# Performance work log

Measured on AMD Instinct MI355X. Metric: run time of the kernel, lower is better.

The kernel has to match this reference:

```python
import jax, jax.numpy as jnp
import numpy as np

N_NODES = 100000
N_EDGES = 800000
IN_FEATS = 128
HIDDEN = 64
SCALE = 0.5 ** 0.5  # sqrt(0.5) residual scale
BN_EPS = 1e-5


def setup_inputs() -> dict:
    key = jax.random.key(0)
    ks = jax.random.split(key, 12)
    return {
        "src": jax.random.randint(ks[0], (N_EDGES,), 0, N_NODES, dtype=jnp.int64)
        if jax.config.jax_enable_x64 else jax.random.randint(ks[0], (N_EDGES,), 0, N_NODES),
        "dst": jax.random.randint(ks[1], (N_EDGES,), 0, N_NODES),
        "x": jax.random.normal(ks[2], (N_NODES, IN_FEATS), dtype=jnp.float32),
        "fc_w": jax.random.normal(ks[3], (IN_FEATS, HIDDEN), dtype=jnp.float32) * 0.05,
        "fc_b": jax.random.normal(ks[4], (HIDDEN,), dtype=jnp.float32) * 0.05,
        "w1": jax.random.normal(ks[5], (HIDDEN, HIDDEN), dtype=jnp.float32) * 0.05,
        "b1": jax.random.normal(ks[6], (HIDDEN,), dtype=jnp.float32) * 0.05,
        "w2": jax.random.normal(ks[7], (HIDDEN, HIDDEN), dtype=jnp.float32) * 0.05,
        "b2": jax.random.normal(ks[8], (HIDDEN,), dtype=jnp.float32) * 0.05,
        "gamma": jax.random.normal(ks[9], (HIDDEN,), dtype=jnp.float32) * 0.05 + 1.0,
        "beta": jax.random.normal(ks[10], (HIDDEN,), dtype=jnp.float32) * 0.05,
    }


def _graph_conv(h, w, b, src, dst, norm_src, norm_dst, n_nodes):
    # DGL GraphConv, norm='both': y = D_in^{-1/2} A D_out^{-1/2} (h W) + b
    h = h @ w                                   # [N, H]
    m = h[src] * norm_src[:, None]              # gather + src-degree norm, [E, H]
    agg = jax.ops.segment_sum(m, dst, num_segments=n_nodes)  # scatter-add, [N, H]
    return agg * norm_dst[:, None] + b


def reference(src, dst, x, fc_w, fc_b, w1, b1, w2, b2, gamma, beta):
    n_nodes = x.shape[0]
    ones_e = jnp.ones(src.shape[0], dtype=x.dtype)
    deg_out = jnp.clip(jax.ops.segment_sum(ones_e, src, num_segments=n_nodes), 1.0)
    deg_in = jnp.clip(jax.ops.segment_sum(ones_e, dst, num_segments=n_nodes), 1.0)
    norm_src = (deg_out ** -0.5)[src]           # per-edge source normalization
    norm_dst = deg_in ** -0.5                   # per-node destination normalization

    h = x @ fc_w + fc_b                          # fc: [N, H]
    h = (h + _graph_conv(h, w1, b1, src, dst, norm_src, norm_dst, n_nodes)) * SCALE
    h = (h + _graph_conv(h, w2, b2, src, dst, norm_src, norm_dst, n_nodes)) * SCALE

    # BatchNorm1d (training-mode batch statistics over nodes, biased variance)
    mu = h.mean(axis=0)
    var = ((h - mu) ** 2).mean(axis=0)
    h = (h - mu) * jax.lax.rsqrt(var + BN_EPS) * gamma + beta
    return h
```

## Files before the change

### kernel.cpp

```cpp
#include <hip/hip_runtime.h>

#define HIDDEN 64
#define INFEAT 128
#define SCALE_C 0.70710678118654752f
#define BN_EPS 1e-5f
#define AGG_GRID 2048
#define RED_BLK 32

__device__ __forceinline__ int rli(int v, int l){ return __builtin_amdgcn_readlane(v, l); }
__device__ __forceinline__ float rlf(float v, int l){
  return __int_as_float(__builtin_amdgcn_readlane(__float_as_int(v), l));
}

template<int KDIM, bool ADDB, bool FUSET>
__device__ __forceinline__ void gemm_body(int bid, const float* __restrict__ X,
    const float* __restrict__ W, const float* __restrict__ B,
    float* __restrict__ Y, const float* __restrict__ W2, float* __restrict__ T, int N)
{
  __shared__ float smem[64 * 65];
  const int tid  = threadIdx.x;
  const int lane = tid & 63;
  const int wid  = __builtin_amdgcn_readfirstlane(tid >> 6);
  const int c0 = wid * 16;
  const int base = bid * 64;
  const int gnode = base + lane;

  float acc[16];
  #pragma unroll
  for (int c = 0; c < 16; ++c) acc[c] = ADDB ? B[c0 + c] : 0.f;

  constexpr int NCHUNK = KDIM / 32;
  #pragma unroll 1
  for (int ck = 0; ck < NCHUNK; ++ck){
    __syncthreads();
    #pragma unroll
    for (int i = 0; i < 2; ++i){
      int f  = i * 256 + tid;
      int nd = f >> 3;
      int kq = f & 7;
      float4 v = make_float4(0.f, 0.f, 0.f, 0.f);
      if (base + nd < N)
        v = *(const float4*)(X + (size_t)(base + nd) * KDIM + ck * 32 + kq * 4);
      float* p = &smem[nd * 65 + kq * 4];
      p[0] = v.x; p[1] = v.y; p[2] = v.z; p[3] = v.w;
    }
    __syncthreads();
    const float* wrow = W + (size_t)ck * 32 * HIDDEN + c0;
    #pragma unroll
    for (int k = 0; k < 32; ++k){
      float xv = smem[lane * 65 + k];
      #pragma unroll
      for (int c = 0; c < 16; ++c)
        acc[c] = fmaf(xv, wrow[k * HIDDEN + c], acc[c]);
    }
  }

  if (gnode < N){
    float4* yp = (float4*)(Y + (size_t)gnode * HIDDEN + c0);
    #pragma unroll
    for (int j = 0; j < 4; ++j)
      yp[j] = make_float4(acc[4*j], acc[4*j+1], acc[4*j+2], acc[4*j+3]);
  }

  if constexpr (FUSET){
    __syncthreads();
    #pragma unroll
    for (int c = 0; c < 16; ++c) smem[lane * 65 + c0 + c] = acc[c];
    __syncthreads();
    float tacc[16];
    #pragma unroll
    for (int c = 0; c < 16; ++c) tacc[c] = 0.f;
    const float* w2r = W2 + c0;
    #pragma unroll
    for (int k = 0; k < 64; ++k){
      float hv = smem[lane * 65 + k];
      #pragma unroll
      for (int c = 0; c < 16; ++c)
        tacc[c] = fmaf(hv, w2r[k * HIDDEN + c], tacc[c]);
    }
    if (gnode < N){
      float4* tp = (float4*)(T + (size_t)gnode * HIDDEN + c0);
      #pragma unroll
      for (int j = 0; j < 4; ++j)
        tp[j] = make_float4(tacc[4*j], tacc[4*j+1], tacc[4*j+2], tacc[4*j+3]);
    }
  }
}

__device__ __forceinline__ int role_gemm_idx(int b, int GB, int TOT, int& histIdx){
  int fb  = (int)(((long)b * GB) / TOT);
  int fb1 = (int)(((long)(b + 1) * GB) / TOT);
  histIdx = b - fb;
  return (fb1 > fb) ? fb : -1;
}

__global__ __launch_bounds__(256) void k_mega1(const int* __restrict__ dst,
    int* __restrict__ degI, int* __restrict__ rank, int E,
    const float* __restrict__ x, const float* __restrict__ fc_w,
    const float* __restrict__ fc_b, float* __restrict__ h,
    const float* __restrict__ w1, float* __restrict__ t, int N, int GB, int TOT){
  int hIdx;
  int g = role_gemm_idx(blockIdx.x, GB, TOT, hIdx);
  if (g >= 0) gemm_body<INFEAT, true, true>(g, x, fc_w, fc_b, h, w1, t, N);
  else {
    int e0 = hIdx * 1024 + threadIdx.x;
    #pragma unroll
    for (int i = 0; i < 4; ++i){
      int e = e0 + i * 256;
      if (e < E) rank[e] = atomicAdd(&degI[dst[e]], 1);
    }
  }
}

__global__ __launch_bounds__(256) void k_place(const int* __restrict__ src,
    const int* __restrict__ dst, const int* __restrict__ rank,
    const int* __restrict__ rp, int* __restrict__ cs, int* __restrict__ degO, int E){
  int e0 = blockIdx.x * 1024 + threadIdx.x;
  #pragma unroll
  for (int i = 0; i < 4; ++i){
    int e = e0 + i * 256;
    if (e < E){
      int s = src[e];
      cs[rp[dst[e]] + rank[e]] = s;
      atomicAdd(&degO[s], 1);
    }
  }
}

__global__ __launch_bounds__(256) void k_gemm64(const float* __restrict__ X,
    const float* __restrict__ W, float* __restrict__ Y, int N){
  gemm_body<HIDDEN, false, false>(blockIdx.x, X, W, nullptr, Y, nullptr, nullptr, N);
}

__global__ void k_scan1(const int* __restrict__ deg, int* __restrict__ bsum, int N){
  __shared__ int sh[256];
  int t = threadIdx.x;
  int i = blockIdx.x * 256 + t;
  sh[t] = (i < N) ? deg[i] : 0;
  __syncthreads();
  for (int ofs = 128; ofs > 0; ofs >>= 1){
    if (t < ofs) sh[t] += sh[t + ofs];
    __syncthreads();
  }
  if (t == 0) bsum[blockIdx.x] = sh[0];
}

__global__ void k_scan2(int* __restrict__ bsum, int NB){
  __shared__ int sh[512];
  int t = threadIdx.x;
  int v = (t < NB) ? bsum[t] : 0;
  sh[t] = v;
  __syncthreads();
  for (int ofs = 1; ofs < 512; ofs <<= 1){
    int u = (t >= ofs) ? sh[t - ofs] : 0;
    __syncthreads();
    sh[t] += u;
    __syncthreads();
  }
  if (t < NB) bsum[t] = sh[t] - v;
}

__global__ void k_scan3(const int* __restrict__ degI, const int* __restrict__ bofs,
                        int* __restrict__ rp, float* __restrict__ norm_in, int N, int E){
  __shared__ int sh[256];
  int t = threadIdx.x;
  int i = blockIdx.x * 256 + t;
  int v = (i < N) ? degI[i] : 0;
  sh[t] = v;
  __syncthreads();
  for (int ofs = 1; ofs < 256; ofs <<= 1){
    int u = (t >= ofs) ? sh[t - ofs] : 0;
    __syncthreads();
    sh[t] += u;
    __syncthreads();
  }
  if (i < N){
    int excl = sh[t] - v + bofs[blockIdx.x];
    rp[i] = excl;
    if (i == N - 1) rp[N] = E;
    norm_in[i] = rsqrtf((float)max(v, 1));
  }
}

template<bool PRE>
__device__ __forceinline__ float gather_row(const int* __restrict__ rp,
    const int* __restrict__ cs, const float* __restrict__ t,
    const int* __restrict__ degO, int n, int lane){
  const int start = rp[n], end = rp[n + 1];
  float acc = 0.f;
  for (int j0 = start; j0 < end; j0 += 64){
    int cnt = end - j0; if (cnt > 64) cnt = 64;
    int sidx = (j0 + lane < end) ? cs[j0 + lane] : 0;
    int d = 0;
    for (; d + 8 <= cnt; d += 8){
      int a0 = rli(sidx, d),   a1 = rli(sidx, d+1);
      int a2 = rli(sidx, d+2), a3 = rli(sidx, d+3);
      int a4 = rli(sidx, d+4), a5 = rli(sidx, d+5);
      int a6 = rli(sidx, d+6), a7 = rli(sidx, d+7);
      float v0 = t[(size_t)a0 * HIDDEN + lane];
      float v1 = t[(size_t)a1 * HIDDEN + lane];
      float v2 = t[(size_t)a2 * HIDDEN + lane];
      float v3 = t[(size_t)a3 * HIDDEN + lane];
      float v4 = t[(size_t)a4 * HIDDEN + lane];
      float v5 = t[(size_t)a5 * HIDDEN + lane];
      float v6 = t[(size_t)a6 * HIDDEN + lane];
      float v7 = t[(size_t)a7 * HIDDEN + lane];
      if (PRE){
        acc += v0; acc += v1; acc += v2; acc += v3;
        acc += v4; acc += v5; acc += v6; acc += v7;
      } else {
        float n0 = rsqrtf((float)degO[a0]);
        float n1 = rsqrtf((float)degO[a1]);
        float n2 = rsqrtf((float)degO[a2]);
        float n3 = rsqrtf((float)degO[a3]);
        float n4 = rsqrtf((float)degO[a4]);
        float n5 = rsqrtf((float)degO[a5]);
        float n6 = rsqrtf((float)degO[a6]);
        float n7 = rsqrtf((float)degO[a7]);
        acc = fmaf(v0, n0, acc); acc = fmaf(v1, n1, acc);
        acc = fmaf(v2, n2, acc); acc = fmaf(v3, n3, acc);
        acc = fmaf(v4, n4, acc); acc = fmaf(v5, n5, acc);
        acc = fmaf(v6, n6, acc); acc = fmaf(v7, n7, acc);
      }
    }
    for (; d < cnt; ++d){
      int a = rli(sidx, d);
      float v = t[(size_t)a * HIDDEN + lane];
      if (PRE) acc += v;
      else     acc = fmaf(v, rsqrtf((float)degO[a]), acc);
    }
  }
  return acc;
}

template<bool BN, bool PRE, bool FUSET2>
__global__ __launch_bounds__(256, 4) void k_agg(const int* __restrict__ rp, const int* __restrict__ cs,
    const float* __restrict__ t, const int* __restrict__ degO,
    const float* __restrict__ norm_in, const float* __restrict__ b,
    const float* __restrict__ w2, float* __restrict__ h,
    float* __restrict__ t2, float* __restrict__ bnpart, int N)
{
  const int tid = threadIdx.x;
  const int lane = tid & 63;
  const int wv = (blockIdx.x * 256 + tid) >> 6;
  const int nw = (gridDim.x * 256) >> 6;
  const float bv = b[lane];
  float s1 = 0.f, s2 = 0.f;

  float w2c[64];
  if constexpr (FUSET2){
    #pragma unroll
    for (int k = 0; k < 64; ++k) w2c[k] = w2[k * HIDDEN + lane];
  }

  for (int n = wv; n < N; n += nw){
    float acc = gather_row<PRE>(rp, cs, t, degO, n, lane);
    size_t idx = (size_t)n * HIDDEN + lane;
    float v = (h[idx] + acc * norm_in[n] + bv) * SCALE_C;
    h[idx] = v;
    if (BN){ s1 += v; s2 += v * v; }
    if constexpr (FUSET2){
      float nout = rsqrtf((float)max(degO[n], 1));
      float ta0 = 0.f, ta1 = 0.f, ta2 = 0.f, ta3 = 0.f;
      #pragma unroll
      for (int k = 0; k < 64; k += 4){
        ta0 = fmaf(rlf(v, k),     w2c[k],     ta0);
        ta1 = fmaf(rlf(v, k + 1), w2c[k + 1], ta1);
        ta2 = fmaf(rlf(v, k + 2), w2c[k + 2], ta2);
        ta3 = fmaf(rlf(v, k + 3), w2c[k + 3], ta3);
      }
      t2[idx] = ((ta0 + ta1) + (ta2 + ta3)) * nout;
    }
  }

  if (BN){
    __shared__ float l1[256], l2[256];
    l1[tid] = s1; l2[tid] = s2;
    __syncthreads();
    if (tid < 64){
      float a1 = l1[tid] + l1[tid+64] + l1[tid+128] + l1[tid+192];
      float a2 = l2[tid] + l2[tid+64] + l2[tid+128] + l2[tid+192];
      bnpart[blockIdx.x * 128 + tid] = a1;
      bnpart[blockIdx.x * 128 + 64 + tid] = a2;
    }
  }
}

__global__ __launch_bounds__(256) void k_bnred(const float* __restrict__ bnpart,
    float* __restrict__ bnred, int nblk){
  int col  = threadIdx.x & 127;
  int half = threadIdx.x >> 7;
  int rows = nblk / RED_BLK;
  int r0 = blockIdx.x * rows;
  float s = 0.f;
  for (int r = half; r < rows; r += 2)
    s += bnpart[(size_t)(r0 + r) * 128 + col];
  __shared__ float sh[256];
  sh[threadIdx.x] = s;
  __syncthreads();
  if (threadIdx.x < 128)
    bnred[blockIdx.x * 128 + threadIdx.x] = sh[threadIdx.x] + sh[threadIdx.x + 128];
}

__global__ void k_bnfin(const float* __restrict__ bnred,
    const float* __restrict__ gamma, const float* __restrict__ beta,
    float* __restrict__ bnab, float invN){
  int c = threadIdx.x;
  float s1 = 0.f, s2 = 0.f;
  #pragma unroll
  for (int b = 0; b < RED_BLK; ++b){ s1 += bnred[b*128 + c]; s2 += bnred[b*128 + 64 + c]; }
  float mu  = s1 * invN;
  float var = s2 * invN - mu * mu;
  float rstd = rsqrtf(var + BN_EPS);
  float sc = gamma[c] * rstd;
  bnab[c] = sc;
  bnab[64 + c] = beta[c] - mu * sc;
}

__global__ void k_bnapply(float* __restrict__ h, const float* __restrict__ bnab, long total4){
  long i = (long)blockIdx.x * blockDim.x + threadIdx.x;
  if (i < total4){
    int c = (int)((i * 4) & 63);
    float4 v = ((float4*)h)[i];
    v.x = fmaf(v.x, bnab[c],     bnab[64 + c]);
    v.y = fmaf(v.y, bnab[c + 1], bnab[65 + c]);
    v.z = fmaf(v.z, bnab[c + 2], bnab[66 + c]);
    v.w = fmaf(v.w, bnab[c + 3], bnab[67 + c]);
    ((float4*)h)[i] = v;
  }
}

extern "C" void kernel_launch(void* const* d_in, const int* in_sizes, int n_in,
                              void* d_out, int out_size, void* d_ws, size_t ws_size,
                              hipStream_t stream){
  const int* src = (const int*)d_in[0];
  const int* dst = (const int*)d_in[1];
  const float* x     = (const float*)d_in[2];
  const float* fc_w  = (const float*)d_in[3];
  const float* fc_b  = (const float*)d_in[4];
  const float* w1    = (const float*)d_in[5];
  const float* b1    = (const float*)d_in[6];
  const float* w2    = (const float*)d_in[7];
  const float* b2    = (const float*)d_in[8];
  const float* gamma = (const float*)d_in[9];
  const float* beta  = (const float*)d_in[10];
  const int E = in_sizes[0];
  const int N = in_sizes[2] / INFEAT;
  const int NB  = (N + 255) / 256;
  const int EB4 = (E + 1023) / 1024;
  const int GB  = (N + 63) / 64;
  const int TOT = EB4 + GB;

  float* h = (float*)d_out;

  const size_t Nh = (size_t)N * HIDDEN;
  size_t need = (2 * Nh + N + (size_t)AGG_GRID * 128 + RED_BLK * 128 + 128) * 4
              + ((size_t)3 * N + 1 + 512 + 2 * (size_t)E) * 4;
  const bool fused = ws_size >= need;

  float* t        = (float*)d_ws;
  float* t2       = fused ? (t + Nh) : nullptr;
  float* norm_in  = fused ? (t2 + Nh) : (t + Nh);
  float* bnpart   = norm_in + N;
  float* bnred    = bnpart + AGG_GRID * 128;
  float* bnab     = bnred + RED_BLK * 128;
  int*   degO     = (int*)(bnab + 128);
  int*   degI     = degO + N;
  int*   rp       = degI + N;
  int*   bsum     = rp + N + 1;
  int*   rank     = bsum + 512;
  int*   cs       = rank + E;

  hipMemsetAsync(degO, 0, 2 * (size_t)N * sizeof(int), stream);

  k_mega1<<<TOT, 256, 0, stream>>>(dst, degI, rank, E,
                                   x, fc_w, fc_b, h, w1, t, N, GB, TOT);

  k_scan1<<<NB, 256, 0, stream>>>(degI, bsum, N);
  k_scan2<<<1, 512, 0, stream>>>(bsum, NB);
  k_scan3<<<NB, 256, 0, stream>>>(degI, bsum, rp, norm_in, N, E);

  k_place<<<EB4, 256, 0, stream>>>(src, dst, rank, rp, cs, degO, E);

  if (fused){
    k_agg<false, false, true><<<AGG_GRID, 256, 0, stream>>>(
        rp, cs, t, degO, norm_in, b1, w2, h, t2, nullptr, N);
    k_agg<true, true, false><<<AGG_GRID, 256, 0, stream>>>(
        rp, cs, t2, degO, norm_in, b2, nullptr, h, nullptr, bnpart, N);
  } else {
    k_agg<false, false, false><<<AGG_GRID, 256, 0, stream>>>(
        rp, cs, t, degO, norm_in, b1, nullptr, h, nullptr, nullptr, N);
    k_gemm64<<<GB, 256, 0, stream>>>(h, w2, t, N);
    k_agg<true, false, false><<<AGG_GRID, 256, 0, stream>>>(
        rp, cs, t, degO, norm_in, b2, nullptr, h, nullptr, bnpart, N);
  }

  k_bnred<<<RED_BLK, 256, 0, stream>>>(bnpart, bnred, AGG_GRID);
  k_bnfin<<<1, 64, 0, stream>>>(bnred, gamma, beta, bnab, 1.0f / (float)N);
  long total4 = (long)N * HIDDEN / 4;
  k_bnapply<<<(int)((total4 + 255) / 256), 256, 0, stream>>>(h, bnab, total4);
}
```

Before: 363.7 us.

## Gather neighbor rows with float4 loads across four edge groups per wave

Restructures the CSR aggregation so each wave splits into four 16-lane groups. Each group loads a full 64-float row as float4 per lane, and the groups walk different edges in parallel before a cross-group shuffle reduction. This replaces per-lane scalar gathers driven by readlane broadcasts, aiming for wider memory transactions and more edges in flight. The cost is extra xor shuffles per node and only one group writing results; the fused second-layer transform now reads the vector components through readlane.

Result: faster. 341.0 us (-6.2%).

```diff
diff --git a/kernel.cpp b/kernel.cpp
--- a/kernel.cpp
+++ b/kernel.cpp
@@ -183,54 +183,51 @@
 }
 
 template<bool PRE>
-__device__ __forceinline__ float gather_row(const int* __restrict__ rp,
+__device__ __forceinline__ float4 gather_row4(const int* __restrict__ rp,
     const int* __restrict__ cs, const float* __restrict__ t,
-    const int* __restrict__ degO, int n, int lane){
+    const int* __restrict__ degO, int n, int g, int s4){
   const int start = rp[n], end = rp[n + 1];
-  float acc = 0.f;
-  for (int j0 = start; j0 < end; j0 += 64){
-    int cnt = end - j0; if (cnt > 64) cnt = 64;
-    int sidx = (j0 + lane < end) ? cs[j0 + lane] : 0;
-    int d = 0;
-    for (; d + 8 <= cnt; d += 8){
-      int a0 = rli(sidx, d),   a1 = rli(sidx, d+1);
-      int a2 = rli(sidx, d+2), a3 = rli(sidx, d+3);
-      int a4 = rli(sidx, d+4), a5 = rli(sidx, d+5);
-      int a6 = rli(sidx, d+6), a7 = rli(sidx, d+7);
-      float v0 = t[(size_t)a0 * HIDDEN + lane];
-      float v1 = t[(size_t)a1 * HIDDEN + lane];
-      float v2 = t[(size_t)a2 * HIDDEN + lane];
-      float v3 = t[(size_t)a3 * HIDDEN + lane];
-      float v4 = t[(size_t)a4 * HIDDEN + lane];
-      float v5 = t[(size_t)a5 * HIDDEN + lane];
-      float v6 = t[(size_t)a6 * HIDDEN + lane];
-      float v7 = t[(size_t)a7 * HIDDEN + lane];
-      if (PRE){
-        acc += v0; acc += v1; acc += v2; acc += v3;
-        acc += v4; acc += v5; acc += v6; acc += v7;
-      } else {
-        float n0 = rsqrtf((float)degO[a0]);
-        float n1 = rsqrtf((float)degO[a1]);
-        float n2 = rsqrtf((float)degO[a2]);
-        float n3 = rsqrtf((float)degO[a3]);
-        float n4 = rsqrtf((float)degO[a4]);
-        float n5 = rsqrtf((float)degO[a5]);
-        float n6 = rsqrtf((float)degO[a6]);
-        float n7 = rsqrtf((float)degO[a7]);
-        acc = fmaf(v0, n0, acc); acc = fmaf(v1, n1, acc);
-        acc = fmaf(v2, n2, acc); acc = fmaf(v3, n3, acc);
-        acc = fmaf(v4, n4, acc); acc = fmaf(v5, n5, acc);
-        acc = fmaf(v6, n6, acc); acc = fmaf(v7, n7, acc);
-      }
-    }
-    for (; d < cnt; ++d){
-      int a = rli(sidx, d);
-      float v = t[(size_t)a * HIDDEN + lane];
-      if (PRE) acc += v;
-      else     acc = fmaf(v, rsqrtf((float)degO[a]), acc);
+  float4 acc = make_float4(0.f, 0.f, 0.f, 0.f);
+  int j = start + g;
+  for (; j + 4 < end; j += 8){
+    int a0 = cs[j], a1 = cs[j + 4];
+    float4 v0 = *(const float4*)(t + (size_t)a0 * HIDDEN + s4);
+    float4 v1 = *(const float4*)(t + (size_t)a1 * HIDDEN + s4);
+    if (PRE){
+      acc.x += v0.x; acc.y += v0.y; acc.z += v0.z; acc.w += v0.w;
+      acc.x += v1.x; acc.y += v1.y; acc.z += v1.z; acc.w += v1.w;
+    } else {
+      float n0 = rsqrtf((float)degO[a0]);
+      float n1 = rsqrtf((float)degO[a1]);
+      acc.x = fmaf(v0.x, n0, acc.x); acc.y = fmaf(v0.y, n0, acc.y);
+      acc.z = fmaf(v0.z, n0, acc.z); acc.w = fmaf(v0.w, n0, acc.w);
+      acc.x = fmaf(v1.x, n1, acc.x); acc.y = fmaf(v1.y, n1, acc.y);
+      acc.z = fmaf(v1.z, n1, acc.z); acc.w = fmaf(v1.w, n1, acc.w);
+    }
+  }
+  if (j < end){
+    int a = cs[j];
+    float4 v = *(const float4*)(t + (size_t)a * HIDDEN + s4);
+    if (PRE){
+      acc.x += v.x; acc.y += v.y; acc.z += v.z; acc.w += v.w;
+    } else {
+      float nn = rsqrtf((float)degO[a]);
+      acc.x = fmaf(v.x, nn, acc.x); acc.y = fmaf(v.y, nn, acc.y);
+      acc.z = fmaf(v.z, nn, acc.z); acc.w = fmaf(v.w, nn, acc.w);
     }
   }
   return acc;
+}
+
+__device__ __forceinline__ float4 xreduce4(float4 a){
+  #pragma unroll
+  for (int m = 16; m <= 32; m <<= 1){
+    a.x += __shfl_xor(a.x, m, 64);
+    a.y += __shfl_xor(a.y, m, 64);
+    a.z += __shfl_xor(a.z, m, 64);
+    a.w += __shfl_xor(a.w, m, 64);
+  }
+  return a;
 }
 
 template<bool BN, bool PRE, bool FUSET2>
@@ -240,12 +237,15 @@
     const float* __restrict__ w2, float* __restrict__ h,
     float* __restrict__ t2, float* __restrict__ bnpart, int N)
 {
-  const int tid = threadIdx.x;
+  const int tid  = threadIdx.x;
   const int lane = tid & 63;
+  const int g    = lane >> 4;
+  const int s    = lane & 15;
+  const int s4   = s * 4;
   const int wv = (blockIdx.x * 256 + tid) >> 6;
   const int nw = (gridDim.x * 256) >> 6;
-  const float bv = b[lane];
-  float s1 = 0.f, s2 = 0.f;
+  const float4 bv = ((const float4*)b)[s];
+  float4 s1 = make_float4(0.f,0.f,0.f,0.f), s2 = make_float4(0.f,0.f,0.f,0.f);
 
   float w2c[64];
   if constexpr (FUSET2){
@@ -254,32 +254,49 @@
   }
 
   for (int n = wv; n < N; n += nw){
-    float acc = gather_row<PRE>(rp, cs, t, degO, n, lane);
-    size_t idx = (size_t)n * HIDDEN + lane;
-    float v = (h[idx] + acc * norm_in[n] + bv) * SCALE_C;
-    h[idx] = v;
-    if (BN){ s1 += v; s2 += v * v; }
+    float4 acc = gather_row4<PRE>(rp, cs, t, degO, n, g, s4);
+    acc = xreduce4(acc);
+    const size_t rowo = (size_t)n * HIDDEN;
+    const float4 hv = *(const float4*)(h + rowo + s4);
+    const float ni = norm_in[n];
+    float4 v;
+    v.x = (hv.x + acc.x * ni + bv.x) * SCALE_C;
+    v.y = (hv.y + acc.y * ni + bv.y) * SCALE_C;
+    v.z = (hv.z + acc.z * ni + bv.z) * SCALE_C;
+    v.w = (hv.w + acc.w * ni + bv.w) * SCALE_C;
+    if (g == 0){
+      *(float4*)(h + rowo + s4) = v;
+      if (BN){
+        s1.x += v.x; s1.y += v.y; s1.z += v.z; s1.w += v.w;
+        s2.x += v.x*v.x; s2.y += v.y*v.y; s2.z += v.z*v.z; s2.w += v.w*v.w;
+      }
+    }
     if constexpr (FUSET2){
       float nout = rsqrtf((float)max(degO[n], 1));
       float ta0 = 0.f, ta1 = 0.f, ta2 = 0.f, ta3 = 0.f;
       #pragma unroll
       for (int k = 0; k < 64; k += 4){
-        ta0 = fmaf(rlf(v, k),     w2c[k],     ta0);
-        ta1 = fmaf(rlf(v, k + 1), w2c[k + 1], ta1);
-        ta2 = fmaf(rlf(v, k + 2), w2c[k + 2], ta2);
-        ta3 = fmaf(rlf(v, k + 3), w2c[k + 3], ta3);
+        const int ln = k >> 2;
+        ta0 = fmaf(rlf(v.x, ln), w2c[k],     ta0);
+        ta1 = fmaf(rlf(v.y, ln), w2c[k + 1], ta1);
+        ta2 = fmaf(rlf(v.z, ln), w2c[k + 2], ta2);
+        ta3 = fmaf(rlf(v.w, ln), w2c[k + 3], ta3);
       }
-      t2[idx] = ((ta0 + ta1) + (ta2 + ta3)) * nout;
+      t2[rowo + lane] = ((ta0 + ta1) + (ta2 + ta3)) * nout;
     }
   }
 
   if (BN){
-    __shared__ float l1[256], l2[256];
-    l1[tid] = s1; l2[tid] = s2;
+    __shared__ float l1[4][64], l2[4][64];
+    const int wid = tid >> 6;
+    if (g == 0){
+      l1[wid][s4+0] = s1.x; l1[wid][s4+1] = s1.y; l1[wid][s4+2] = s1.z; l1[wid][s4+3] = s1.w;
+      l2[wid][s4+0] = s2.x; l2[wid][s4+1] = s2.y; l2[wid][s4+2] = s2.z; l2[wid][s4+3] = s2.w;
+    }
     __syncthreads();
     if (tid < 64){
-      float a1 = l1[tid] + l1[tid+64] + l1[tid+128] + l1[tid+192];
-      float a2 = l2[tid] + l2[tid+64] + l2[tid+128] + l2[tid+192];
+      float a1 = l1[0][tid] + l1[1][tid] + l1[2][tid] + l1[3][tid];
+      float a2 = l2[0][tid] + l2[1][tid] + l2[2][tid] + l2[3][tid];
       bnpart[blockIdx.x * 128 + tid] = a1;
       bnpart[blockIdx.x * 128 + 64 + tid] = a2;
     }
```
